# Kernel tuning notes

Hardware: AMD Instinct MI355X
Metric: run time of the kernel (lower is better)

The kernel has to match this reference:

```python
import jax, jax.numpy as jnp
import numpy as np

D_MODEL = 1024
N_HEADS = 16
HEAD_DIM = D_MODEL // N_HEADS


def setup_inputs() -> dict:
    key = jax.random.key(0)
    ks = jax.random.split(key, 10)
    B, S = 4, 2048
    scale = 1.0 / np.sqrt(D_MODEL)
    inp = {
        "x": jax.random.normal(ks[0], (B, S, D_MODEL), dtype=jnp.float32),
        "attention_mask": jnp.ones((B, S), dtype=jnp.int32),
        "Wq": jax.random.normal(ks[1], (D_MODEL, D_MODEL), dtype=jnp.float32) * scale,
        "bq": jnp.zeros((D_MODEL,), dtype=jnp.float32),
        "Wk": jax.random.normal(ks[2], (D_MODEL, D_MODEL), dtype=jnp.float32) * scale,
        "bk": jnp.zeros((D_MODEL,), dtype=jnp.float32),
        "Wv": jax.random.normal(ks[3], (D_MODEL, D_MODEL), dtype=jnp.float32) * scale,
        "bv": jnp.zeros((D_MODEL,), dtype=jnp.float32),
        "Wo": jax.random.normal(ks[4], (D_MODEL, D_MODEL), dtype=jnp.float32) * scale,
        "bo": jnp.zeros((D_MODEL,), dtype=jnp.float32),
    }
    return inp


def reference(x, attention_mask, Wq, bq, Wk, bk, Wv, bv, Wo, bo):
    B, S, _ = x.shape
    # projections, then split heads: [B, H, S, Dh]
    def proj(W, b):
        return (x @ W.T + b).reshape(B, S, N_HEADS, HEAD_DIM).transpose(0, 2, 1, 3)
    Q = proj(Wq, bq)
    K = proj(Wk, bk)
    V = proj(Wv, bv)
    # scores: [B, H, S, S]
    scores = jnp.einsum("bhqd,bhkd->bhqk", Q, K) / np.sqrt(HEAD_DIM)
    mask = attention_mask[:, None, None, :]  # [B,1,1,S]
    scores = jnp.where(mask == 0, -jnp.inf, scores)
    attn = jax.nn.softmax(scores, axis=-1)
    out = jnp.einsum("bhqk,bhkd->bhqd", attn, V)
    out = out.transpose(0, 2, 1, 3).reshape(B, S, D_MODEL)
    out = out @ Wo.T + bo
    return out
```

## Files before the change

### kernel.cpp

```cpp
#include <hip/hip_runtime.h>
#include <stdint.h>
#include <stddef.h>

typedef __attribute__((ext_vector_type(8))) short bf16x8;
typedef __attribute__((ext_vector_type(4))) float f32x4;

#define LOG2E 1.44269504088896340736f

__device__ __forceinline__ unsigned short f2bf(float f) {
  union { float f; unsigned u; } v; v.f = f;
  unsigned u = v.u + 0x7fffu + ((v.u >> 16) & 1u);
  return (unsigned short)(u >> 16);
}

__device__ __forceinline__ void gload_lds16(const void* g, void* l) {
  __builtin_amdgcn_global_load_lds(
      (const __attribute__((address_space(1))) unsigned int*)g,
      (__attribute__((address_space(3))) unsigned int*)l, 16, 0, 0);
}

__global__ void convert_all(const float* __restrict__ x,
                            const float* __restrict__ wq, const float* __restrict__ wk,
                            const float* __restrict__ wv, const float* __restrict__ wo,
                            unsigned short* __restrict__ dst) {
  size_t i = ((size_t)blockIdx.x * 256 + threadIdx.x) * 4;
  const float* src; size_t off;
  if (i < 8388608) { src = x; off = i; }
  else {
    size_t j = i - 8388608;
    int w = (int)(j >> 20);
    off = j & 1048575;
    src = (w == 0) ? wq : (w == 1) ? wk : (w == 2) ? wv : wo;
  }
  const float4 v = *(const float4*)(src + off);
  ushort4 o;
  o.x = f2bf(v.x); o.y = f2bf(v.y); o.z = f2bf(v.z); o.w = f2bf(v.w);
  *(ushort4*)(dst + i) = o;
}

template<int MODE>
__global__ __launch_bounds__(256, 2)
void gemm_bt(const unsigned short* __restrict__ A,
             const unsigned short* __restrict__ Bw,
             const float* __restrict__ bias,
             unsigned short* __restrict__ outb,
             float* __restrict__ outf,
             float scale) {
  __shared__ char lds[32768];
  const int t = threadIdx.x;
  const int lane = t & 63;
  const int wave = t >> 6;
  const int wr = wave >> 1, wc = wave & 1;
  const int bm = blockIdx.y << 7;
  const int bn = blockIdx.x << 7;

  f32x4 acc[4][4];
  for (int i = 0; i < 4; ++i)
    for (int j = 0; j < 4; ++j)
      for (int r = 0; r < 4; ++r) acc[i][j][r] = 0.f;

  for (int kt = 0; kt < 16; ++kt) {
    __syncthreads();
    {
      const size_t abase = ((size_t)bm * 1024 + (size_t)kt * 64) * 2;
      const size_t bbase = ((size_t)bn * 1024 + (size_t)kt * 64) * 2;
      for (int c = 0; c < 4; ++c) {
        const int o = (c << 12) + (t << 4);
        const int r = o >> 7;
        const int kb = o & 127;
        const int kbg = kb ^ ((r & 7) << 4);
        gload_lds16((const char*)A + abase + (size_t)r * 2048 + kbg, lds + o);
      }
      for (int c = 0; c < 4; ++c) {
        const int o = (c << 12) + (t << 4);
        const int r = o >> 7;
        const int kb = o & 127;
        const int kbg = kb ^ ((r & 7) << 4);
        gload_lds16((const char*)Bw + bbase + (size_t)r * 2048 + kbg, lds + 16384 + o);
      }
    }
    __syncthreads();
    for (int ks = 0; ks < 2; ++ks) {
      const int kbl = (ks << 6) + ((lane >> 4) << 4);
      bf16x8 af[4], bfr[4];
      for (int mf = 0; mf < 4; ++mf) {
        const int r = (wr << 6) + (mf << 4) + (lane & 15);
        af[mf] = *(const bf16x8*)(lds + (r << 7) + (kbl ^ ((r & 7) << 4)));
      }
      for (int nf = 0; nf < 4; ++nf) {
        const int r = (wc << 6) + (nf << 4) + (lane & 15);
        bfr[nf] = *(const bf16x8*)(lds + 16384 + (r << 7) + (kbl ^ ((r & 7) << 4)));
      }
      for (int mf = 0; mf < 4; ++mf)
        for (int nf = 0; nf < 4; ++nf)
          acc[mf][nf] = __builtin_amdgcn_mfma_f32_16x16x32_bf16(af[mf], bfr[nf], acc[mf][nf], 0, 0, 0);
    }
  }

  const int rsub = (lane >> 4) << 2;
  const int csub = lane & 15;
  for (int mf = 0; mf < 4; ++mf)
    for (int nf = 0; nf < 4; ++nf) {
      const int row0 = bm + (wr << 6) + (mf << 4) + rsub;
      const int col  = bn + (wc << 6) + (nf << 4) + csub;
      for (int rg = 0; rg < 4; ++rg) {
        const int row = row0 + rg;
        float v = acc[mf][nf][rg];
        if (MODE == 0) {
          v = (v + bias[col]) * scale;
          const int b = row >> 11, s = row & 2047, h = col >> 6, d = col & 63;
          size_t idx = ((size_t)((b << 4) + h) << 11) + (size_t)s;
          idx = (idx << 6) + (size_t)d;
          outb[idx] = f2bf(v);
        } else if (MODE == 2) {
          v = v + bias[row];
          const int b = col >> 11, s = col & 2047;
          const size_t idx = ((size_t)(b * 1024 + row) << 11) + (size_t)s;
          outb[idx] = f2bf(v);
        } else {
          v = v + bias[col];
          outf[(size_t)row * 1024 + (size_t)col] = v;
        }
      }
    }
}

__global__ __launch_bounds__(256, 2)
void attn_fwd(const unsigned short* __restrict__ Q,
              const unsigned short* __restrict__ K,
              const unsigned short* __restrict__ Vt,
              const int* __restrict__ mask,
              unsigned short* __restrict__ Aout) {
  __shared__ char lds[65536];
  const int t = threadIdx.x, lane = t & 63, wave = t >> 6;
  const int blk = blockIdx.x;
  const int head = blk & 63, qt = blk >> 6;
  const int b = head >> 4, h = head & 15;
  const int qbase = qt << 7;
  const unsigned short* Qh = Q + ((size_t)head << 17);
  const unsigned short* Kh = K + ((size_t)head << 17);
  const unsigned short* Vh = Vt + ((size_t)head << 17);
  const int* maskb = mask + (b << 11);

  bf16x8 aq[2][2];
  for (int rf = 0; rf < 2; ++rf)
    for (int ks = 0; ks < 2; ++ks) {
      const int row = qbase + (wave << 5) + (rf << 4) + (lane & 15);
      const int k = (ks << 5) + ((lane >> 4) << 3);
      aq[rf][ks] = *(const bf16x8*)(Qh + ((size_t)row << 6) + (size_t)k);
    }

  f32x4 oacc[2][4];
  for (int i = 0; i < 2; ++i)
    for (int j = 0; j < 4; ++j)
      for (int r = 0; r < 4; ++r) oacc[i][j][r] = 0.f;
  float lsum[2][4];
  for (int i = 0; i < 2; ++i)
    for (int r = 0; r < 4; ++r) lsum[i][r] = 0.f;

  char* Plds = lds + 32768 + (wave << 13);

  for (int it = 0; it < 16; ++it) {
    const int kv = it << 7;
    __syncthreads();
    for (int c = 0; c < 4; ++c) {
      const int o = (c << 12) + (t << 4);
      const int r = o >> 7, kb = o & 127;
      gload_lds16((const char*)Kh + (((size_t)(kv + r)) << 7) + (size_t)(kb ^ ((r & 7) << 4)),
                  lds + o);
    }
    for (int c = 0; c < 4; ++c) {
      const int o = (c << 12) + (t << 4);
      const int d = o >> 8, kb = o & 255;
      gload_lds16((const char*)Vh + (((size_t)d) << 12) + (size_t)(kv << 1)
                      + (size_t)(kb ^ ((d & 7) << 4)),
                  lds + 16384 + o);
    }
    __syncthreads();

    float ma[8];
    for (int cf = 0; cf < 8; ++cf)
      ma[cf] = maskb[kv + (cf << 4) + (lane & 15)] ? 0.f : -1e30f;

    f32x4 s[2][8];
    for (int i = 0; i < 2; ++i)
      for (int j = 0; j < 8; ++j)
        for (int r = 0; r < 4; ++r) s[i][j][r] = 0.f;
    for (int ks = 0; ks < 2; ++ks) {
      const int kbl = (ks << 6) + ((lane >> 4) << 4);
      bf16x8 bk[8];
      for (int cf = 0; cf < 8; ++cf) {
        const int r = (cf << 4) + (lane & 15);
        bk[cf] = *(const bf16x8*)(lds + (r << 7) + (kbl ^ ((r & 7) << 4)));
      }
      for (int rf = 0; rf < 2; ++rf)
        for (int cf = 0; cf < 8; ++cf)
          s[rf][cf] = __builtin_amdgcn_mfma_f32_16x16x32_bf16(aq[rf][ks], bk[cf], s[rf][cf], 0, 0, 0);
    }

    for (int rf = 0; rf < 2; ++rf)
      for (int cf = 0; cf < 8; ++cf) {
        const int colb = (cf << 5) + ((lane & 15) << 1);
        for (int rg = 0; rg < 4; ++rg) {
          const float p = __builtin_amdgcn_exp2f(s[rf][cf][rg] + ma[cf]);
          lsum[rf][rg] += p;
          const int q = (rf << 4) + ((lane >> 4) << 2) + rg;
          *(unsigned short*)(Plds + (q << 8) + (colb ^ ((q & 7) << 4))) = f2bf(p);
        }
      }

    for (int ks = 0; ks < 4; ++ks) {
      const int kbl = (ks << 6) + ((lane >> 4) << 4);
      bf16x8 ap[2], bv[4];
      for (int rf = 0; rf < 2; ++rf) {
        const int q = (rf << 4) + (lane & 15);
        ap[rf] = *(const bf16x8*)(Plds + (q << 8) + (kbl ^ ((q & 7) << 4)));
      }
      for (int cf = 0; cf < 4; ++cf) {
        const int d = (cf << 4) + (lane & 15);
        bv[cf] = *(const bf16x8*)(lds + 16384 + (d << 8) + (kbl ^ ((d & 7) << 4)));
      }
      for (int rf = 0; rf < 2; ++rf)
        for (int cf = 0; cf < 4; ++cf)
          oacc[rf][cf] = __builtin_amdgcn_mfma_f32_16x16x32_bf16(ap[rf], bv[cf], oacc[rf][cf], 0, 0, 0);
    }
  }

  for (int rf = 0; rf < 2; ++rf)
    for (int rg = 0; rg < 4; ++rg) {
      float ls = lsum[rf][rg];
      ls += __shfl_xor(ls, 1);
      ls += __shfl_xor(ls, 2);
      ls += __shfl_xor(ls, 4);
      ls += __shfl_xor(ls, 8);
      const float inv = 1.f / ls;
      for (int cf = 0; cf < 4; ++cf) oacc[rf][cf][rg] *= inv;
    }

  for (int rf = 0; rf < 2; ++rf)
    for (int cf = 0; cf < 4; ++cf)
      for (int rg = 0; rg < 4; ++rg) {
        const int q = qbase + (wave << 5) + (rf << 4) + ((lane >> 4) << 2) + rg;
        const int d = (cf << 4) + (lane & 15);
        Aout[(((size_t)(b << 11) + q) << 10) + (size_t)((h << 6) + d)] = f2bf(oacc[rf][cf][rg]);
      }
}

extern "C" void kernel_launch(void* const* d_in, const int* in_sizes, int n_in,
                              void* d_out, int out_size, void* d_ws, size_t ws_size,
                              hipStream_t stream) {
  const float* x  = (const float*)d_in[0];
  const int* mask = (const int*)d_in[1];
  const float* Wq = (const float*)d_in[2];
  const float* bq = (const float*)d_in[3];
  const float* Wk = (const float*)d_in[4];
  const float* bk = (const float*)d_in[5];
  const float* Wv = (const float*)d_in[6];
  const float* bv = (const float*)d_in[7];
  const float* Wo = (const float*)d_in[8];
  const float* bo = (const float*)d_in[9];
  float* out = (float*)d_out;

  unsigned short* xb  = (unsigned short*)d_ws;
  unsigned short* wqb = xb  + 8388608;
  unsigned short* wkb = wqb + 1048576;
  unsigned short* wvb = wkb + 1048576;
  unsigned short* wob = wvb + 1048576;
  unsigned short* Qb  = wob + 1048576;
  unsigned short* Kb  = Qb  + 8388608;
  unsigned short* Vtb = Kb  + 8388608;
  unsigned short* Ab  = Vtb + 8388608;

  convert_all<<<12288, 256, 0, stream>>>(x, Wq, Wk, Wv, Wo, xb);
  const float qscale = 0.125f * LOG2E;
  gemm_bt<0><<<dim3(8, 64), 256, 0, stream>>>(xb, wqb, bq, Qb, nullptr, qscale);
  gemm_bt<0><<<dim3(8, 64), 256, 0, stream>>>(xb, wkb, bk, Kb, nullptr, 1.0f);
  gemm_bt<2><<<dim3(64, 8), 256, 0, stream>>>(wvb, xb, bv, Vtb, nullptr, 1.0f);
  attn_fwd<<<1024, 256, 0, stream>>>(Qb, Kb, Vtb, mask, Ab);
  gemm_bt<3><<<dim3(8, 64), 256, 0, stream>>>(Ab, wob, bo, nullptr, out, 1.0f);
}
```

Before: 316.8 us.

## Keep attention probabilities in registers via transposed QK and permlane swaps

The QK^T MFMA now uses swapped operands, so each lane holds S^T fragments. Probabilities are packed to bf16 with v_cvt_pk_bf16_f32 and rearranged with permlane32/permlane16 swaps directly into PV A-operand layout, which removes the per-wave P round trip through LDS and halves LDS to 32KB. The mask is precomputed as an additive float array in the convert kernel and loaded as float4. s_setprio is added around the MFMA blocks in the GEMM and attention kernels. This relies on the exact gfx950 permlane lane mapping being correct.

Result: faster. 283.0 us (-10.7%).

```diff
diff --git a/kernel.cpp b/kernel.cpp
--- a/kernel.cpp
+++ b/kernel.cpp
@@ -19,11 +19,36 @@
       (__attribute__((address_space(3))) unsigned int*)l, 16, 0, 0);
 }
 
+__device__ __forceinline__ unsigned cvt_pk_bf16(float lo, float hi) {
+  unsigned r;
+  asm("v_cvt_pk_bf16_f32 %0, %1, %2" : "=v"(r) : "v"(lo), "v"(hi));
+  return r;
+}
+__device__ __forceinline__ void pl32_swap(unsigned& a, unsigned& b) {
+  asm("v_permlane32_swap_b32 %0, %1" : "+v"(a), "+v"(b));
+}
+__device__ __forceinline__ void pl16_swap(unsigned& a, unsigned& b) {
+  asm("v_permlane16_swap_b32 %0, %1" : "+v"(a), "+v"(b));
+}
+
 __global__ void convert_all(const float* __restrict__ x,
                             const float* __restrict__ wq, const float* __restrict__ wk,
                             const float* __restrict__ wv, const float* __restrict__ wo,
-                            unsigned short* __restrict__ dst) {
+                            const int* __restrict__ mask,
+                            unsigned short* __restrict__ dst,
+                            float* __restrict__ addm) {
   size_t i = ((size_t)blockIdx.x * 256 + threadIdx.x) * 4;
+  if (i >= 12582912) {
+    size_t j = i - 12582912;
+    const int4 m = *(const int4*)(mask + j);
+    float4 o;
+    o.x = m.x ? 0.f : -1e30f;
+    o.y = m.y ? 0.f : -1e30f;
+    o.z = m.z ? 0.f : -1e30f;
+    o.w = m.w ? 0.f : -1e30f;
+    *(float4*)(addm + j) = o;
+    return;
+  }
   const float* src; size_t off;
   if (i < 8388608) { src = x; off = i; }
   else {
@@ -91,9 +116,11 @@
         const int r = (wc << 6) + (nf << 4) + (lane & 15);
         bfr[nf] = *(const bf16x8*)(lds + 16384 + (r << 7) + (kbl ^ ((r & 7) << 4)));
       }
+      __builtin_amdgcn_s_setprio(1);
       for (int mf = 0; mf < 4; ++mf)
         for (int nf = 0; nf < 4; ++nf)
           acc[mf][nf] = __builtin_amdgcn_mfma_f32_16x16x32_bf16(af[mf], bfr[nf], acc[mf][nf], 0, 0, 0);
+      __builtin_amdgcn_s_setprio(0);
     }
   }
 
@@ -129,10 +156,11 @@
 void attn_fwd(const unsigned short* __restrict__ Q,
               const unsigned short* __restrict__ K,
               const unsigned short* __restrict__ Vt,
-              const int* __restrict__ mask,
+              const float* __restrict__ addm,
               unsigned short* __restrict__ Aout) {
-  __shared__ char lds[65536];
+  __shared__ char lds[32768];
   const int t = threadIdx.x, lane = t & 63, wave = t >> 6;
+  const int g = lane >> 4, m15 = lane & 15;
   const int blk = blockIdx.x;
   const int head = blk & 63, qt = blk >> 6;
   const int b = head >> 4, h = head & 15;
@@ -140,13 +168,13 @@
   const unsigned short* Qh = Q + ((size_t)head << 17);
   const unsigned short* Kh = K + ((size_t)head << 17);
   const unsigned short* Vh = Vt + ((size_t)head << 17);
-  const int* maskb = mask + (b << 11);
+  const float* amb = addm + (b << 11);
 
   bf16x8 aq[2][2];
   for (int rf = 0; rf < 2; ++rf)
     for (int ks = 0; ks < 2; ++ks) {
-      const int row = qbase + (wave << 5) + (rf << 4) + (lane & 15);
-      const int k = (ks << 5) + ((lane >> 4) << 3);
+      const int row = qbase + (wave << 5) + (rf << 4) + m15;
+      const int k = (ks << 5) + (g << 3);
       aq[rf][ks] = *(const bf16x8*)(Qh + ((size_t)row << 6) + (size_t)k);
     }
 
@@ -154,11 +182,7 @@
   for (int i = 0; i < 2; ++i)
     for (int j = 0; j < 4; ++j)
       for (int r = 0; r < 4; ++r) oacc[i][j][r] = 0.f;
-  float lsum[2][4];
-  for (int i = 0; i < 2; ++i)
-    for (int r = 0; r < 4; ++r) lsum[i][r] = 0.f;
-
-  char* Plds = lds + 32768 + (wave << 13);
+  float lsum[2] = {0.f, 0.f};
 
   for (int it = 0; it < 16; ++it) {
     const int kv = it << 7;
@@ -178,70 +202,84 @@
     }
     __syncthreads();
 
-    float ma[8];
+    float4 fm[8];
     for (int cf = 0; cf < 8; ++cf)
-      ma[cf] = maskb[kv + (cf << 4) + (lane & 15)] ? 0.f : -1e30f;
+      fm[cf] = *(const float4*)(amb + kv + (cf << 4) + (g << 2));
 
     f32x4 s[2][8];
     for (int i = 0; i < 2; ++i)
       for (int j = 0; j < 8; ++j)
         for (int r = 0; r < 4; ++r) s[i][j][r] = 0.f;
     for (int ks = 0; ks < 2; ++ks) {
-      const int kbl = (ks << 6) + ((lane >> 4) << 4);
+      const int kbl = (ks << 6) + (g << 4);
       bf16x8 bk[8];
       for (int cf = 0; cf < 8; ++cf) {
-        const int r = (cf << 4) + (lane & 15);
+        const int r = (cf << 4) + m15;
         bk[cf] = *(const bf16x8*)(lds + (r << 7) + (kbl ^ ((r & 7) << 4)));
       }
+      __builtin_amdgcn_s_setprio(1);
       for (int rf = 0; rf < 2; ++rf)
         for (int cf = 0; cf < 8; ++cf)
-          s[rf][cf] = __builtin_amdgcn_mfma_f32_16x16x32_bf16(aq[rf][ks], bk[cf], s[rf][cf], 0, 0, 0);
-    }
-
-    for (int rf = 0; rf < 2; ++rf)
-      for (int cf = 0; cf < 8; ++cf) {
-        const int colb = (cf << 5) + ((lane & 15) << 1);
+          s[rf][cf] = __builtin_amdgcn_mfma_f32_16x16x32_bf16(bk[cf], aq[rf][ks], s[rf][cf], 0, 0, 0);
+      __builtin_amdgcn_s_setprio(0);
+    }
+
+    bf16x8 pa[2][4];
+    for (int rf = 0; rf < 2; ++rf) {
+      for (int cf = 0; cf < 8; ++cf)
         for (int rg = 0; rg < 4; ++rg) {
-          const float p = __builtin_amdgcn_exp2f(s[rf][cf][rg] + ma[cf]);
-          lsum[rf][rg] += p;
-          const int q = (rf << 4) + ((lane >> 4) << 2) + rg;
-          *(unsigned short*)(Plds + (q << 8) + (colb ^ ((q & 7) << 4))) = f2bf(p);
+          const float p = __builtin_amdgcn_exp2f(s[rf][cf][rg] + fm[cf][rg]);
+          lsum[rf] += p;
+          s[rf][cf][rg] = p;
         }
-      }
-
-    for (int ks = 0; ks < 4; ++ks) {
-      const int kbl = (ks << 6) + ((lane >> 4) << 4);
-      bf16x8 ap[2], bv[4];
-      for (int rf = 0; rf < 2; ++rf) {
-        const int q = (rf << 4) + (lane & 15);
-        ap[rf] = *(const bf16x8*)(Plds + (q << 8) + (kbl ^ ((q & 7) << 4)));
-      }
+      for (int k2 = 0; k2 < 4; ++k2) {
+        const int ce = k2 << 1, co = ce + 1;
+        unsigned A = cvt_pk_bf16(s[rf][ce][0], s[rf][ce][1]);
+        unsigned B = cvt_pk_bf16(s[rf][ce][2], s[rf][ce][3]);
+        unsigned C = cvt_pk_bf16(s[rf][co][0], s[rf][co][1]);
+        unsigned D = cvt_pk_bf16(s[rf][co][2], s[rf][co][3]);
+        pl32_swap(A, C);
+        pl32_swap(B, D);
+        pl16_swap(A, C);
+        pl16_swap(B, D);
+        union { unsigned u[4]; bf16x8 v; } pk;
+        pk.u[0] = A; pk.u[1] = B; pk.u[2] = C; pk.u[3] = D;
+        pa[rf][k2] = pk.v;
+      }
+    }
+
+    for (int k2 = 0; k2 < 4; ++k2) {
+      const int kbl = (k2 << 6) + (g << 4);
+      bf16x8 bv[4];
       for (int cf = 0; cf < 4; ++cf) {
-        const int d = (cf << 4) + (lane & 15);
+        const int d = (cf << 4) + m15;
         bv[cf] = *(const bf16x8*)(lds + 16384 + (d << 8) + (kbl ^ ((d & 7) << 4)));
       }
+      __builtin_amdgcn_s_setprio(1);
       for (int rf = 0; rf < 2; ++rf)
         for (int cf = 0; cf < 4; ++cf)
-          oacc[rf][cf] = __builtin_amdgcn_mfma_f32_16x16x32_bf16(ap[rf], bv[cf], oacc[rf][cf], 0, 0, 0);
-    }
-  }
-
-  for (int rf = 0; rf < 2; ++rf)
-    for (int rg = 0; rg < 4; ++rg) {
-      float ls = lsum[rf][rg];
-      ls += __shfl_xor(ls, 1);
-      ls += __shfl_xor(ls, 2);
-      ls += __shfl_xor(ls, 4);
-      ls += __shfl_xor(ls, 8);
-      const float inv = 1.f / ls;
-      for (int cf = 0; cf < 4; ++cf) oacc[rf][cf][rg] *= inv;
-    }
+          oacc[rf][cf] = __builtin_amdgcn_mfma_f32_16x16x32_bf16(pa[rf][k2], bv[cf], oacc[rf][cf], 0, 0, 0);
+      __builtin_amdgcn_s_setprio(0);
+    }
+  }
+
+  for (int rf = 0; rf < 2; ++rf) {
+    float ls = lsum[rf];
+    ls += __shfl_xor(ls, 16);
+    ls += __shfl_xor(ls, 32);
+    float inv[4];
+    for (int rg = 0; rg < 4; ++rg)
+      inv[rg] = 1.f / __shfl(ls, (g << 2) + rg);
+    for (int cf = 0; cf < 4; ++cf)
+      for (int rg = 0; rg < 4; ++rg)
+        oacc[rf][cf][rg] *= inv[rg];
+  }
 
   for (int rf = 0; rf < 2; ++rf)
     for (int cf = 0; cf < 4; ++cf)
       for (int rg = 0; rg < 4; ++rg) {
-        const int q = qbase + (wave << 5) + (rf << 4) + ((lane >> 4) << 2) + rg;
-        const int d = (cf << 4) + (lane & 15);
+        const int q = qbase + (wave << 5) + (rf << 4) + (g << 2) + rg;
+        const int d = (cf << 4) + m15;
         Aout[(((size_t)(b << 11) + q) << 10) + (size_t)((h << 6) + d)] = f2bf(oacc[rf][cf][rg]);
       }
 }
@@ -270,12 +308,13 @@
   unsigned short* Kb  = Qb  + 8388608;
   unsigned short* Vtb = Kb  + 8388608;
   unsigned short* Ab  = Vtb + 8388608;
-
-  convert_all<<<12288, 256, 0, stream>>>(x, Wq, Wk, Wv, Wo, xb);
+  float* addm = (float*)(Ab + 8388608);
+
+  convert_all<<<12296, 256, 0, stream>>>(x, Wq, Wk, Wv, Wo, mask, xb, addm);
   const float qscale = 0.125f * LOG2E;
   gemm_bt<0><<<dim3(8, 64), 256, 0, stream>>>(xb, wqb, bq, Qb, nullptr, qscale);
   gemm_bt<0><<<dim3(8, 64), 256, 0, stream>>>(xb, wkb, bk, Kb, nullptr, 1.0f);
   gemm_bt<2><<<dim3(64, 8), 256, 0, stream>>>(wvb, xb, bv, Vtb, nullptr, 1.0f);
-  attn_fwd<<<1024, 256, 0, stream>>>(Qb, Kb, Vtb, mask, Ab);
+  attn_fwd<<<1024, 256, 0, stream>>>(Qb, Kb, Vtb, addm, Ab);
   gemm_bt<3><<<dim3(8, 64), 256, 0, stream>>>(Ab, wob, bo, nullptr, out, 1.0f);
 }
```
